# Performance work log

Measured on AMD Instinct MI355X. Metric: run time of the kernel, lower is better.

## Reference

```python
import jax, jax.numpy as jnp
import numpy as np

E, B, S, D, F = 8, 8, 2048, 1024, 4096  # experts, batch, seq, d_model, d_expert
LANG_BASE = 4  # lang codes 4..11 map to experts 0..7 (codes <=3 are non-routed specials)


def setup_inputs() -> dict:
    key = jax.random.key(0)
    k = jax.random.split(key, 5)
    hidden_states = jax.random.normal(k[0], (B, S, D), jnp.float32)
    w1 = jax.random.normal(k[1], (E, D, F), jnp.float32) * (1.0 / np.sqrt(D))
    w3 = jax.random.normal(k[2], (E, D, F), jnp.float32) * (1.0 / np.sqrt(D))
    w2 = jax.random.normal(k[3], (E, F, D), jnp.float32) * (1.0 / np.sqrt(F))
    langs = jax.random.randint(k[4], (B, 1), LANG_BASE, LANG_BASE + E)
    return {"hidden_states": hidden_states, "w1": w1, "w2": w2, "w3": w3, "langs": langs}


def reference(hidden_states, w1, w2, w3, langs):
    # routing_weights = 1 / (#langs > 3 per row), with inf -> 1 when no routed lang
    cnt = (langs > 3).sum(axis=-1)
    rw = jnp.where(cnt == 0, 1.0, 1.0 / jnp.maximum(cnt, 1)).astype(hidden_states.dtype)
    # one lang per row -> exactly one expert per batch row; gather its weights
    e_idx = langs[:, 0] - LANG_BASE  # [B]
    W1 = w1[e_idx]  # [B, D, F]
    W3 = w3[e_idx]  # [B, D, F]
    W2 = w2[e_idx]  # [B, F, D]
    a = jnp.einsum('bsd,bdf->bsf', hidden_states, W1)
    b = jnp.einsum('bsd,bdf->bsf', hidden_states, W3)
    h = jax.nn.gelu(a, approximate=False) * b
    out = jnp.einsum('bsf,bfd->bsd', h, W2)
    return out * rw[:, None, None]
```

## Files before the change

kernel.cpp:

```cpp
#include <hip/hip_runtime.h>
#include <hip/hip_bf16.h>
#include <stdint.h>

#define E_ 8
#define B_ 8
#define S_ 2048
#define D_ 1024
#define F_ 4096

typedef short short8 __attribute__((ext_vector_type(8)));
typedef float f32x4  __attribute__((ext_vector_type(4)));
typedef unsigned short u16;

union U16x8 { uint4 v; u16 s[8]; };
union U16x4 { uint2 v; u16 s[4]; };

__device__ __forceinline__ float gelu_exact(float x) {
    return 0.5f * x * (1.0f + erff(x * 0.70710678118654752f));
}
__device__ __forceinline__ u16 f2b(float v) {
    __hip_bfloat16 b = __float2bfloat16(v);
    return *(const u16*)&b;
}

__device__ __forceinline__ void gload_lds16(const u16* g, u16* l) {
    __builtin_amdgcn_global_load_lds(
        (const __attribute__((address_space(1))) uint32_t*)g,
        (__attribute__((address_space(3))) uint32_t*)l, 16, 0, 0);
}

__global__ void convert_x(const float* __restrict__ X, u16* __restrict__ Xb) {
    const size_t i = ((size_t)blockIdx.x * 256 + threadIdx.x) * 8;
    const float4 v0 = *(const float4*)(X + i);
    const float4 v1 = *(const float4*)(X + i + 4);
    U16x8 o;
    o.s[0] = f2b(v0.x); o.s[1] = f2b(v0.y); o.s[2] = f2b(v0.z); o.s[3] = f2b(v0.w);
    o.s[4] = f2b(v1.x); o.s[5] = f2b(v1.y); o.s[6] = f2b(v1.z); o.s[7] = f2b(v1.w);
    *(uint4*)(Xb + i) = o.v;
}

__global__ void transpose_w(const float* __restrict__ src, u16* __restrict__ dst,
                            int R, int C) {
    __shared__ u16 tile[64 * 72];
    const int c0 = blockIdx.x * 64;
    const int r0 = blockIdx.y * 64;
    const size_t base = (size_t)blockIdx.z * R * C;
    const int t  = threadIdx.x;
    const int rr = t >> 4;
    const int cc = (t & 15) * 4;
#pragma unroll
    for (int p = 0; p < 4; ++p) {
        const int r = rr + p * 16;
        const float4 v = *(const float4*)(src + base + (size_t)(r0 + r) * C + c0 + cc);
        tile[(cc + 0) * 72 + r] = f2b(v.x);
        tile[(cc + 1) * 72 + r] = f2b(v.y);
        tile[(cc + 2) * 72 + r] = f2b(v.z);
        tile[(cc + 3) * 72 + r] = f2b(v.w);
    }
    __syncthreads();
    const int cn = t >> 2;
    const int ch = (t & 3) * 4;
#pragma unroll
    for (int p = 0; p < 4; ++p) {
        const int rch = ch + p * 16;
        *(uint2*)(dst + base + (size_t)(c0 + cn) * R + r0 + rch) =
            *(const uint2*)(tile + cn * 72 + rch);
    }
}

__global__ __launch_bounds__(256, 2)
void gateup_v2(const u16* __restrict__ Xb, const u16* __restrict__ W1t,
               const u16* __restrict__ W3t, const int* __restrict__ langs,
               u16* __restrict__ H)
{
    __shared__ u16 sX [128 * 64];
    __shared__ u16 sW1[ 64 * 64];
    __shared__ u16 sW3[ 64 * 64];

    const int f0 = blockIdx.x * 64;
    const int s0 = blockIdx.y * 128;
    const int b  = blockIdx.z;
    const int e  = (langs[b] - 4) & 7;

    const int t    = threadIdx.x;
    const int lane = t & 63;
    const int w    = t >> 6;
    const int wr   = w >> 1, wc = w & 1;
    const int lm   = lane & 15;
    const int lq   = lane >> 4;
    const int lr   = lane >> 3;
    const int lcg  = (lane & 7) ^ lr;
    const int hsw  = lm & 7;

    f32x4 acc1[4][2], acc2[4][2];
#pragma unroll
    for (int i = 0; i < 4; ++i)
#pragma unroll
        for (int j = 0; j < 2; ++j) {
            acc1[i][j] = (f32x4){0.f, 0.f, 0.f, 0.f};
            acc2[i][j] = (f32x4){0.f, 0.f, 0.f, 0.f};
        }

    const size_t xbase = ((size_t)b * S_ + s0) * D_;
    const size_t wbase = ((size_t)e * F_ + f0) * D_;
    const u16* xg  = Xb  + xbase + (size_t)(w * 32 + lr) * D_ + lcg * 8;
    const u16* w1g = W1t + wbase + (size_t)(w * 16 + lr) * D_ + lcg * 8;
    const u16* w3g = W3t + wbase + (size_t)(w * 16 + lr) * D_ + lcg * 8;

    for (int kt = 0; kt < D_ / 64; ++kt) {
        const int k0 = kt * 64;
        __syncthreads();
#pragma unroll
        for (int i = 0; i < 4; ++i)
            gload_lds16(xg + (size_t)i * 8 * D_ + k0, sX + (w * 32 + i * 8) * 64);
#pragma unroll
        for (int i = 0; i < 2; ++i) {
            gload_lds16(w1g + (size_t)i * 8 * D_ + k0, sW1 + (w * 16 + i * 8) * 64);
            gload_lds16(w3g + (size_t)i * 8 * D_ + k0, sW3 + (w * 16 + i * 8) * 64);
        }
        __syncthreads();

#pragma unroll
        for (int kk = 0; kk < 64; kk += 32) {
            const int cgb = kk >> 3;
            short8 a[4], b1[2], b3[2];
#pragma unroll
            for (int i = 0; i < 4; ++i) {
                const int r = wr * 64 + i * 16 + lm;
                a[i] = *(const short8*)(sX + r * 64 + (((cgb + lq) ^ hsw) << 3));
            }
#pragma unroll
            for (int j = 0; j < 2; ++j) {
                const int n = wc * 32 + j * 16 + lm;
                b1[j] = *(const short8*)(sW1 + n * 64 + (((cgb + lq) ^ hsw) << 3));
                b3[j] = *(const short8*)(sW3 + n * 64 + (((cgb + lq) ^ hsw) << 3));
            }
#pragma unroll
            for (int i = 0; i < 4; ++i)
#pragma unroll
                for (int j = 0; j < 2; ++j) {
                    acc1[i][j] = __builtin_amdgcn_mfma_f32_16x16x32_bf16(a[i], b1[j], acc1[i][j], 0, 0, 0);
                    acc2[i][j] = __builtin_amdgcn_mfma_f32_16x16x32_bf16(a[i], b3[j], acc2[i][j], 0, 0, 0);
                }
        }
    }

#pragma unroll
    for (int i = 0; i < 4; ++i)
#pragma unroll
        for (int j = 0; j < 2; ++j)
#pragma unroll
            for (int r = 0; r < 4; ++r) {
                const int row = wr * 64 + i * 16 + lq * 4 + r;
                const int col = wc * 32 + j * 16 + lm;
                const float hv = gelu_exact(acc1[i][j][r]) * acc2[i][j][r];
                H[((size_t)b * S_ + s0 + row) * F_ + f0 + col] = f2b(hv);
            }
}

__global__ __launch_bounds__(256, 2)
void down_v2(const u16* __restrict__ H, const u16* __restrict__ W2t,
             const int* __restrict__ langs, float* __restrict__ Y)
{
    __shared__ u16 sH[128 * 64];
    __shared__ u16 sW[128 * 64];

    const int d0 = blockIdx.x * 128;
    const int s0 = blockIdx.y * 128;
    const int b  = blockIdx.z;
    const int e  = (langs[b] - 4) & 7;

    const int t    = threadIdx.x;
    const int lane = t & 63;
    const int w    = t >> 6;
    const int wr   = w >> 1, wc = w & 1;
    const int lm   = lane & 15;
    const int lq   = lane >> 4;
    const int lr   = lane >> 3;
    const int lcg  = (lane & 7) ^ lr;
    const int hsw  = lm & 7;

    f32x4 acc[4][4];
#pragma unroll
    for (int i = 0; i < 4; ++i)
#pragma unroll
        for (int j = 0; j < 4; ++j) acc[i][j] = (f32x4){0.f, 0.f, 0.f, 0.f};

    const size_t hbase = ((size_t)b * S_ + s0) * F_;
    const size_t wbase = ((size_t)e * D_ + d0) * F_;
    const u16* hg = H   + hbase + (size_t)(w * 32 + lr) * F_ + lcg * 8;
    const u16* wg = W2t + wbase + (size_t)(w * 32 + lr) * F_ + lcg * 8;

    for (int kt = 0; kt < F_ / 64; ++kt) {
        const int k0 = kt * 64;
        __syncthreads();
#pragma unroll
        for (int i = 0; i < 4; ++i)
            gload_lds16(hg + (size_t)i * 8 * F_ + k0, sH + (w * 32 + i * 8) * 64);
#pragma unroll
        for (int i = 0; i < 4; ++i)
            gload_lds16(wg + (size_t)i * 8 * F_ + k0, sW + (w * 32 + i * 8) * 64);
        __syncthreads();

#pragma unroll
        for (int kk = 0; kk < 64; kk += 32) {
            const int cgb = kk >> 3;
            short8 a[4], bb[4];
#pragma unroll
            for (int i = 0; i < 4; ++i) {
                const int r = wr * 64 + i * 16 + lm;
                a[i] = *(const short8*)(sH + r * 64 + (((cgb + lq) ^ hsw) << 3));
            }
#pragma unroll
            for (int j = 0; j < 4; ++j) {
                const int n = wc * 64 + j * 16 + lm;
                bb[j] = *(const short8*)(sW + n * 64 + (((cgb + lq) ^ hsw) << 3));
            }
#pragma unroll
            for (int i = 0; i < 4; ++i)
#pragma unroll
                for (int j = 0; j < 4; ++j)
                    acc[i][j] = __builtin_amdgcn_mfma_f32_16x16x32_bf16(a[i], bb[j], acc[i][j], 0, 0, 0);
        }
    }

#pragma unroll
    for (int i = 0; i < 4; ++i)
#pragma unroll
        for (int j = 0; j < 4; ++j)
#pragma unroll
            for (int r = 0; r < 4; ++r) {
                const int row = wr * 64 + i * 16 + lq * 4 + r;
                const int col = wc * 64 + j * 16 + lm;
                Y[((size_t)b * S_ + s0 + row) * D_ + d0 + col] = acc[i][j][r];
            }
}

__device__ __forceinline__ U16x8 load8f(const float* p, size_t off) {
    U16x8 r;
    const float4 v0 = *(const float4*)(p + off);
    const float4 v1 = *(const float4*)(p + off + 4);
    r.s[0] = f2b(v0.x); r.s[1] = f2b(v0.y); r.s[2] = f2b(v0.z); r.s[3] = f2b(v0.w);
    r.s[4] = f2b(v1.x); r.s[5] = f2b(v1.y); r.s[6] = f2b(v1.z); r.s[7] = f2b(v1.w);
    return r;
}

__global__ __launch_bounds__(256, 2)
void gateup_fb(const float* __restrict__ X, const float* __restrict__ W1,
               const float* __restrict__ W3, const int* __restrict__ langs,
               u16* __restrict__ H, int s_off, int schunk)
{
    __shared__ u16 sX [128 * 72];
    __shared__ u16 sW1[ 64 * 72];
    __shared__ u16 sW3[ 64 * 72];
    const int f0 = blockIdx.x * 64;
    const int sl = blockIdx.y * 128;
    const int b  = blockIdx.z;
    const int e  = (langs[b] - 4) & 7;
    const int t = threadIdx.x, lane = t & 63, w = t >> 6;
    const int wr = w >> 1, wc = w & 1, lm = lane & 15, lq = lane >> 4;
    const int wsel = t >> 7, idx = t & 127;
    const int wn = (idx & 7) * 8, wk = (idx >> 3) * 4;
    const float* Wsrc = wsel ? W3 : W1;
    u16* sWdst = wsel ? sW3 : sW1;

    f32x4 acc1[4][2], acc2[4][2];
#pragma unroll
    for (int i = 0; i < 4; ++i)
#pragma unroll
        for (int j = 0; j < 2; ++j) {
            acc1[i][j] = (f32x4){0.f,0.f,0.f,0.f};
            acc2[i][j] = (f32x4){0.f,0.f,0.f,0.f};
        }
    const size_t xbase = ((size_t)b * S_ + s_off + sl) * D_;
    const size_t wbase = (size_t)e * D_ * F_ + f0;
    for (int kt = 0; kt < D_ / 64; ++kt) {
        const int k0 = kt * 64;
        U16x8 xr[4], rr[4];
#pragma unroll
        for (int i = 0; i < 4; ++i) {
            const int ch = t + i * 256, row = ch >> 3, kk = (ch & 7) * 8;
            xr[i] = load8f(X, xbase + (size_t)row * D_ + k0 + kk);
        }
#pragma unroll
        for (int r = 0; r < 4; ++r)
            rr[r] = load8f(Wsrc, wbase + (size_t)(k0 + wk + r) * F_ + wn);
        __syncthreads();
#pragma unroll
        for (int i = 0; i < 4; ++i) {
            const int ch = t + i * 256, row = ch >> 3, kk = (ch & 7) * 8;
            *(uint4*)(sX + row * 72 + kk) = xr[i].v;
        }
#pragma unroll
        for (int j = 0; j < 8; ++j) {
            U16x4 o;
            o.s[0] = rr[0].s[j]; o.s[1] = rr[1].s[j];
            o.s[2] = rr[2].s[j]; o.s[3] = rr[3].s[j];
            *(uint2*)(sWdst + (wn + j) * 72 + wk) = o.v;
        }
        __syncthreads();
#pragma unroll
        for (int kk = 0; kk < 64; kk += 32) {
            short8 a[4], b1[2], b3[2];
#pragma unroll
            for (int i = 0; i < 4; ++i)
                a[i] = *(const short8*)(sX + (wr * 64 + i * 16 + lm) * 72 + kk + lq * 8);
#pragma unroll
            for (int j = 0; j < 2; ++j) {
                b1[j] = *(const short8*)(sW1 + (wc * 32 + j * 16 + lm) * 72 + kk + lq * 8);
                b3[j] = *(const short8*)(sW3 + (wc * 32 + j * 16 + lm) * 72 + kk + lq * 8);
            }
#pragma unroll
            for (int i = 0; i < 4; ++i)
#pragma unroll
                for (int j = 0; j < 2; ++j) {
                    acc1[i][j] = __builtin_amdgcn_mfma_f32_16x16x32_bf16(a[i], b1[j], acc1[i][j], 0, 0, 0);
                    acc2[i][j] = __builtin_amdgcn_mfma_f32_16x16x32_bf16(a[i], b3[j], acc2[i][j], 0, 0, 0);
                }
        }
    }
#pragma unroll
    for (int i = 0; i < 4; ++i)
#pragma unroll
        for (int j = 0; j < 2; ++j)
#pragma unroll
            for (int r = 0; r < 4; ++r) {
                const int row = wr * 64 + i * 16 + lq * 4 + r;
                const int col = wc * 32 + j * 16 + lm;
                H[((size_t)b * schunk + sl + row) * F_ + f0 + col] =
                    f2b(gelu_exact(acc1[i][j][r]) * acc2[i][j][r]);
            }
}

__global__ __launch_bounds__(256, 2)
void down_fb(const u16* __restrict__ Hm, const float* __restrict__ W2,
             const int* __restrict__ langs, float* __restrict__ Y,
             int s_off, int schunk)
{
    __shared__ u16 sH[128 * 72];
    __shared__ u16 sW[128 * 72];
    const int d0 = blockIdx.x * 128;
    const int sl = blockIdx.y * 128;
    const int b  = blockIdx.z;
    const int e  = (langs[b] - 4) & 7;
    const int t = threadIdx.x, lane = t & 63, w = t >> 6;
    const int wr = w >> 1, wc = w & 1, lm = lane & 15, lq = lane >> 4;
    const int wn = (t & 15) * 8, wk = (t >> 4) * 4;

    f32x4 acc[4][4];
#pragma unroll
    for (int i = 0; i < 4; ++i)
#pragma unroll
        for (int j = 0; j < 4; ++j) acc[i][j] = (f32x4){0.f,0.f,0.f,0.f};
    const size_t hbase = ((size_t)b * schunk + sl) * F_;
    const size_t wbase = (size_t)e * F_ * D_ + d0;
    for (int kt = 0; kt < F_ / 64; ++kt) {
        const int k0 = kt * 64;
        U16x8 hr[4], rr[4];
#pragma unroll
        for (int i = 0; i < 4; ++i) {
            const int ch = t + i * 256, row = ch >> 3, kk = (ch & 7) * 8;
            hr[i].v = *(const uint4*)(Hm + hbase + (size_t)row * F_ + k0 + kk);
        }
#pragma unroll
        for (int r = 0; r < 4; ++r)
            rr[r] = load8f(W2, wbase + (size_t)(k0 + wk + r) * D_ + wn);
        __syncthreads();
#pragma unroll
        for (int i = 0; i < 4; ++i) {
            const int ch = t + i * 256, row = ch >> 3, kk = (ch & 7) * 8;
            *(uint4*)(sH + row * 72 + kk) = hr[i].v;
        }
#pragma unroll
        for (int j = 0; j < 8; ++j) {
            U16x4 o;
            o.s[0] = rr[0].s[j]; o.s[1] = rr[1].s[j];
            o.s[2] = rr[2].s[j]; o.s[3] = rr[3].s[j];
            *(uint2*)(sW + (wn + j) * 72 + wk) = o.v;
        }
        __syncthreads();
#pragma unroll
        for (int kk = 0; kk < 64; kk += 32) {
            short8 a[4], bb[4];
#pragma unroll
            for (int i = 0; i < 4; ++i)
                a[i] = *(const short8*)(sH + (wr * 64 + i * 16 + lm) * 72 + kk + lq * 8);
#pragma unroll
            for (int j = 0; j < 4; ++j)
                bb[j] = *(const short8*)(sW + (wc * 64 + j * 16 + lm) * 72 + kk + lq * 8);
#pragma unroll
            for (int i = 0; i < 4; ++i)
#pragma unroll
                for (int j = 0; j < 4; ++j)
                    acc[i][j] = __builtin_amdgcn_mfma_f32_16x16x32_bf16(a[i], bb[j], acc[i][j], 0, 0, 0);
        }
    }
#pragma unroll
    for (int i = 0; i < 4; ++i)
#pragma unroll
        for (int j = 0; j < 4; ++j)
#pragma unroll
            for (int r = 0; r < 4; ++r) {
                const int row = wr * 64 + i * 16 + lq * 4 + r;
                const int col = wc * 64 + j * 16 + lm;
                Y[((size_t)b * S_ + s_off + sl + row) * D_ + d0 + col] = acc[i][j][r];
            }
}

extern "C" void kernel_launch(void* const* d_in, const int* in_sizes, int n_in,
                              void* d_out, int out_size, void* d_ws, size_t ws_size,
                              hipStream_t stream) {
    const float* X  = (const float*)d_in[0];
    const float* W1 = (const float*)d_in[1];
    const float* W2 = (const float*)d_in[2];
    const float* W3 = (const float*)d_in[3];
    const int* langs = (const int*)d_in[4];
    float* Y = (float*)d_out;

    const size_t szXb = (size_t)B_ * S_ * D_ * 2;
    const size_t szW  = (size_t)E_ * F_ * D_ * 2;
    const size_t szH  = (size_t)B_ * S_ * F_ * 2;
    const size_t need = szXb + 2 * szW + szH;

    if (ws_size >= need) {
        u16* Xb  = (u16*)d_ws;
        u16* W1t = (u16*)((char*)d_ws + szXb);
        u16* W3t = (u16*)((char*)d_ws + szXb + szW);
        u16* W2t = W1t;
        u16* Hb  = (u16*)((char*)d_ws + szXb + 2 * szW);

        convert_x<<<(B_ * S_ * D_) / (256 * 8), 256, 0, stream>>>(X, Xb);
        dim3 gt1(F_ / 64, D_ / 64, E_);
        transpose_w<<<gt1, 256, 0, stream>>>(W1, W1t, D_, F_);
        transpose_w<<<gt1, 256, 0, stream>>>(W3, W3t, D_, F_);
        dim3 g1(F_ / 64, S_ / 128, B_);
        gateup_v2<<<g1, 256, 0, stream>>>(Xb, W1t, W3t, langs, Hb);
        dim3 gt2(D_ / 64, F_ / 64, E_);
        transpose_w<<<gt2, 256, 0, stream>>>(W2, W2t, F_, D_);
        dim3 g2(D_ / 128, S_ / 128, B_);
        down_v2<<<g2, 256, 0, stream>>>(Hb, W2t, langs, Y);
    } else {
        u16* H = (u16*)d_ws;
        const size_t slab = (size_t)B_ * F_ * 2 * 128;
        int nslabs = (int)(ws_size / slab);
        if (nslabs < 1) nslabs = 1;
        if (nslabs > S_ / 128) nslabs = S_ / 128;
        const int SCH = nslabs * 128;
        for (int s0 = 0; s0 < S_; s0 += SCH) {
            const int rows = (S_ - s0 < SCH) ? (S_ - s0) : SCH;
            dim3 g1(F_ / 64, rows / 128, B_);
            gateup_fb<<<g1, 256, 0, stream>>>(X, W1, W3, langs, H, s0, SCH);
            dim3 g2(D_ / 128, rows / 128, B_);
            down_fb<<<g2, 256, 0, stream>>>(H, W2, langs, Y, s0, SCH);
        }
    }
}
```

Measured before the change: 867.9 us.

## Rewrite gate-up and down GEMMs with larger tiles and double-buffered LDS pipeline

After: 890.0 us. 1.03x slower.

```diff
diff --git a/kernel.cpp b/kernel.cpp
--- a/kernel.cpp
+++ b/kernel.cpp
@@ -28,6 +28,12 @@
         (const __attribute__((address_space(1))) uint32_t*)g,
         (__attribute__((address_space(3))) uint32_t*)l, 16, 0, 0);
 }
+
+#define SBAR asm volatile("s_barrier" ::: "memory")
+#define WLG0 asm volatile("s_waitcnt lgkmcnt(0)" ::: "memory")
+#define WVM8 asm volatile("s_waitcnt vmcnt(8)" ::: "memory")
+#define WVM4 asm volatile("s_waitcnt vmcnt(4)" ::: "memory")
+#define WVM0 asm volatile("s_waitcnt vmcnt(0)" ::: "memory")
 
 __global__ void convert_x(const float* __restrict__ X, u16* __restrict__ Xb) {
     const size_t i = ((size_t)blockIdx.x * 256 + threadIdx.x) * 8;
@@ -68,17 +74,15 @@
     }
 }
 
-__global__ __launch_bounds__(256, 2)
-void gateup_v2(const u16* __restrict__ Xb, const u16* __restrict__ W1t,
+
+__global__ __launch_bounds__(512, 2)
+void gateup_v3(const u16* __restrict__ Xb, const u16* __restrict__ W1t,
                const u16* __restrict__ W3t, const int* __restrict__ langs,
                u16* __restrict__ H)
 {
-    __shared__ u16 sX [128 * 64];
-    __shared__ u16 sW1[ 64 * 64];
-    __shared__ u16 sW3[ 64 * 64];
-
-    const int f0 = blockIdx.x * 64;
-    const int s0 = blockIdx.y * 128;
+    __shared__ u16 lds[65536];
+    const int f0 = blockIdx.x * 128;
+    const int s0 = blockIdx.y * 256;
     const int b  = blockIdx.z;
     const int e  = (langs[b] - 4) & 7;
 
@@ -86,154 +90,205 @@
     const int lane = t & 63;
     const int w    = t >> 6;
     const int wr   = w >> 1, wc = w & 1;
-    const int lm   = lane & 15;
-    const int lq   = lane >> 4;
-    const int lr   = lane >> 3;
-    const int lcg  = (lane & 7) ^ lr;
-    const int hsw  = lm & 7;
-
-    f32x4 acc1[4][2], acc2[4][2];
+    const int lm   = lane & 15, lq = lane >> 4;
+    const int sr   = lane >> 2, sg = lane & 3;
+
+    const u16* xg   = Xb + ((size_t)b * S_ + s0 + w * 32 + sr) * D_ + sg * 8;
+    const u16* bsrc = (w < 4 ? W1t : W3t)
+                    + ((size_t)e * F_ + f0 + (w & 3) * 32 + sr) * D_ + sg * 8;
+    const int aofs = w * 1024;
+    const int bofs = 16384 + (w >> 2) * 4096 + (w & 3) * 1024;
+
+    f32x4 acc1[4][4], acc2[4][4];
 #pragma unroll
     for (int i = 0; i < 4; ++i)
 #pragma unroll
-        for (int j = 0; j < 2; ++j) {
+        for (int j = 0; j < 4; ++j) {
             acc1[i][j] = (f32x4){0.f, 0.f, 0.f, 0.f};
             acc2[i][j] = (f32x4){0.f, 0.f, 0.f, 0.f};
         }
-
-    const size_t xbase = ((size_t)b * S_ + s0) * D_;
-    const size_t wbase = ((size_t)e * F_ + f0) * D_;
-    const u16* xg  = Xb  + xbase + (size_t)(w * 32 + lr) * D_ + lcg * 8;
-    const u16* w1g = W1t + wbase + (size_t)(w * 16 + lr) * D_ + lcg * 8;
-    const u16* w3g = W3t + wbase + (size_t)(w * 16 + lr) * D_ + lcg * 8;
-
-    for (int kt = 0; kt < D_ / 64; ++kt) {
-        const int k0 = kt * 64;
-        __syncthreads();
-#pragma unroll
-        for (int i = 0; i < 4; ++i)
-            gload_lds16(xg + (size_t)i * 8 * D_ + k0, sX + (w * 32 + i * 8) * 64);
-#pragma unroll
-        for (int i = 0; i < 2; ++i) {
-            gload_lds16(w1g + (size_t)i * 8 * D_ + k0, sW1 + (w * 16 + i * 8) * 64);
-            gload_lds16(w3g + (size_t)i * 8 * D_ + k0, sW3 + (w * 16 + i * 8) * 64);
-        }
-        __syncthreads();
-
-#pragma unroll
-        for (int kk = 0; kk < 64; kk += 32) {
-            const int cgb = kk >> 3;
-            short8 a[4], b1[2], b3[2];
-#pragma unroll
-            for (int i = 0; i < 4; ++i) {
-                const int r = wr * 64 + i * 16 + lm;
-                a[i] = *(const short8*)(sX + r * 64 + (((cgb + lq) ^ hsw) << 3));
+    short8 a[2], b1[4], b3[4];
+
+#define GU_STA(bf, kh, kt) do { \
+    gload_lds16(xg + (size_t)(kt) * 64 + (kh) * 32, \
+                lds + (bf) * 32768 + (kh) * 8192 + aofs); \
+    gload_lds16(xg + (size_t)16 * D_ + (size_t)(kt) * 64 + (kh) * 32, \
+                lds + (bf) * 32768 + (kh) * 8192 + aofs + 512); } while (0)
+#define GU_STB(bf, kh, kt) do { \
+    gload_lds16(bsrc + (size_t)(kt) * 64 + (kh) * 32, \
+                lds + (bf) * 32768 + (kh) * 8192 + bofs); \
+    gload_lds16(bsrc + (size_t)16 * D_ + (size_t)(kt) * 64 + (kh) * 32, \
+                lds + (bf) * 32768 + (kh) * 8192 + bofs + 512); } while (0)
+#define GU_RD(bf, kh, qi, LOADB) do { \
+    const u16* ab_ = lds + (bf) * 32768 + (kh) * 8192; \
+    _Pragma("unroll") \
+    for (int i2 = 0; i2 < 2; ++i2) \
+        a[i2] = *(const short8*)(ab_ + (wr * 64 + (qi) * 32 + i2 * 16 + lm) * 32 + lq * 8); \
+    if (LOADB) { \
+        const u16* bb_ = ab_ + 16384; \
+        _Pragma("unroll") \
+        for (int j = 0; j < 4; ++j) { \
+            b1[j] = *(const short8*)(bb_ + (wc * 64 + j * 16 + lm) * 32 + lq * 8); \
+            b3[j] = *(const short8*)(bb_ + 4096 + (wc * 64 + j * 16 + lm) * 32 + lq * 8); \
+        } } } while (0)
+#define GU_MM(qi) do { \
+    __builtin_amdgcn_s_setprio(1); \
+    _Pragma("unroll") \
+    for (int i2 = 0; i2 < 2; ++i2) \
+    _Pragma("unroll") \
+    for (int j = 0; j < 4; ++j) { \
+        acc1[(qi)*2 + i2][j] = __builtin_amdgcn_mfma_f32_16x16x32_bf16(a[i2], b1[j], acc1[(qi)*2 + i2][j], 0, 0, 0); \
+        acc2[(qi)*2 + i2][j] = __builtin_amdgcn_mfma_f32_16x16x32_bf16(a[i2], b3[j], acc2[(qi)*2 + i2][j], 0, 0, 0); \
+    } \
+    __builtin_amdgcn_s_setprio(0); } while (0)
+#define GU_PH(bf, kh, qi, LOADB, STG, WT) do { \
+    GU_RD(bf, kh, qi, LOADB); STG; SBAR; GU_MM(qi); WT; WLG0; SBAR; } while (0)
+
+    GU_STA(0, 0, 0); GU_STB(0, 0, 0);
+    GU_STA(0, 1, 0); GU_STB(0, 1, 0);
+    GU_STA(1, 0, 1); GU_STB(1, 0, 1);
+    WVM8; SBAR;
+
+#pragma unroll 1
+    for (int u = 0; u < D_ / 128 - 1; ++u) {
+        const int T1 = 2 * u + 1, TN = 2 * u + 2;
+        GU_PH(0, 0, 0, 1, GU_STA(1, 1, T1), );
+        GU_PH(0, 0, 1, 0, GU_STB(1, 1, T1), WVM8);
+        GU_PH(0, 1, 0, 1, GU_STA(0, 0, TN), );
+        GU_PH(0, 1, 1, 0, GU_STB(0, 0, TN), WVM8);
+        GU_PH(1, 0, 0, 1, GU_STA(0, 1, TN), );
+        GU_PH(1, 0, 1, 0, GU_STB(0, 1, TN), WVM8);
+        GU_PH(1, 1, 0, 1, GU_STA(1, 0, TN + 1), );
+        GU_PH(1, 1, 1, 0, GU_STB(1, 0, TN + 1), WVM8);
+    }
+    GU_PH(0, 0, 0, 1, GU_STA(1, 1, D_ / 64 - 1), );
+    GU_PH(0, 0, 1, 0, GU_STB(1, 1, D_ / 64 - 1), WVM8);
+    GU_PH(0, 1, 0, 1, , );
+    GU_PH(0, 1, 1, 0, , WVM4);
+    GU_PH(1, 0, 0, 1, , );
+    GU_PH(1, 0, 1, 0, , WVM0);
+    GU_PH(1, 1, 0, 1, , );
+    GU_PH(1, 1, 1, 0, , );
+
+#pragma unroll
+    for (int fi = 0; fi < 4; ++fi)
+#pragma unroll
+        for (int j = 0; j < 4; ++j)
+#pragma unroll
+            for (int r = 0; r < 4; ++r) {
+                const int row = s0 + wr * 64 + fi * 16 + lq * 4 + r;
+                const int col = f0 + wc * 64 + j * 16 + lm;
+                H[((size_t)b * S_ + row) * F_ + col] =
+                    f2b(gelu_exact(acc1[fi][j][r]) * acc2[fi][j][r]);
             }
-#pragma unroll
-            for (int j = 0; j < 2; ++j) {
-                const int n = wc * 32 + j * 16 + lm;
-                b1[j] = *(const short8*)(sW1 + n * 64 + (((cgb + lq) ^ hsw) << 3));
-                b3[j] = *(const short8*)(sW3 + n * 64 + (((cgb + lq) ^ hsw) << 3));
-            }
-#pragma unroll
-            for (int i = 0; i < 4; ++i)
-#pragma unroll
-                for (int j = 0; j < 2; ++j) {
-                    acc1[i][j] = __builtin_amdgcn_mfma_f32_16x16x32_bf16(a[i], b1[j], acc1[i][j], 0, 0, 0);
-                    acc2[i][j] = __builtin_amdgcn_mfma_f32_16x16x32_bf16(a[i], b3[j], acc2[i][j], 0, 0, 0);
-                }
-        }
-    }
-
-#pragma unroll
-    for (int i = 0; i < 4; ++i)
-#pragma unroll
-        for (int j = 0; j < 2; ++j)
-#pragma unroll
-            for (int r = 0; r < 4; ++r) {
-                const int row = wr * 64 + i * 16 + lq * 4 + r;
-                const int col = wc * 32 + j * 16 + lm;
-                const float hv = gelu_exact(acc1[i][j][r]) * acc2[i][j][r];
-                H[((size_t)b * S_ + s0 + row) * F_ + f0 + col] = f2b(hv);
-            }
-}
-
-__global__ __launch_bounds__(256, 2)
-void down_v2(const u16* __restrict__ H, const u16* __restrict__ W2t,
+#undef GU_STA
+#undef GU_STB
+#undef GU_RD
+#undef GU_MM
+#undef GU_PH
+}
+
+__global__ __launch_bounds__(512, 2)
+void down_v3(const u16* __restrict__ H, const u16* __restrict__ W2t,
              const int* __restrict__ langs, float* __restrict__ Y)
 {
-    __shared__ u16 sH[128 * 64];
-    __shared__ u16 sW[128 * 64];
-
-    const int d0 = blockIdx.x * 128;
-    const int s0 = blockIdx.y * 128;
+    __shared__ u16 lds[65536];
+    const int d0 = blockIdx.x * 256;
+    const int s0 = blockIdx.y * 256;
     const int b  = blockIdx.z;
     const int e  = (langs[b] - 4) & 7;
 
     const int t    = threadIdx.x;
     const int lane = t & 63;
     const int w    = t >> 6;
-    const int wr   = w >> 1, wc = w & 1;
-    const int lm   = lane & 15;
-    const int lq   = lane >> 4;
-    const int lr   = lane >> 3;
-    const int lcg  = (lane & 7) ^ lr;
-    const int hsw  = lm & 7;
-
-    f32x4 acc[4][4];
-#pragma unroll
-    for (int i = 0; i < 4; ++i)
+    const int wr   = w >> 2, wc = w & 3;
+    const int lm   = lane & 15, lq = lane >> 4;
+    const int sr   = lane >> 2, sg = lane & 3;
+
+    const u16* ha = H   + ((size_t)b * S_ + s0 + w * 32 + sr) * F_ + sg * 8;
+    const u16* wa = W2t + ((size_t)e * D_ + d0 + w * 32 + sr) * F_ + sg * 8;
+    const int aofs = w * 1024;
+
+    f32x4 acc[8][4];
+#pragma unroll
+    for (int i = 0; i < 8; ++i)
 #pragma unroll
         for (int j = 0; j < 4; ++j) acc[i][j] = (f32x4){0.f, 0.f, 0.f, 0.f};
-
-    const size_t hbase = ((size_t)b * S_ + s0) * F_;
-    const size_t wbase = ((size_t)e * D_ + d0) * F_;
-    const u16* hg = H   + hbase + (size_t)(w * 32 + lr) * F_ + lcg * 8;
-    const u16* wg = W2t + wbase + (size_t)(w * 32 + lr) * F_ + lcg * 8;
-
-    for (int kt = 0; kt < F_ / 64; ++kt) {
-        const int k0 = kt * 64;
-        __syncthreads();
-#pragma unroll
-        for (int i = 0; i < 4; ++i)
-            gload_lds16(hg + (size_t)i * 8 * F_ + k0, sH + (w * 32 + i * 8) * 64);
-#pragma unroll
-        for (int i = 0; i < 4; ++i)
-            gload_lds16(wg + (size_t)i * 8 * F_ + k0, sW + (w * 32 + i * 8) * 64);
-        __syncthreads();
-
-#pragma unroll
-        for (int kk = 0; kk < 64; kk += 32) {
-            const int cgb = kk >> 3;
-            short8 a[4], bb[4];
-#pragma unroll
-            for (int i = 0; i < 4; ++i) {
-                const int r = wr * 64 + i * 16 + lm;
-                a[i] = *(const short8*)(sH + r * 64 + (((cgb + lq) ^ hsw) << 3));
+    short8 a[4], bb[4];
+
+#define DN_STA(bf, kh, kt) do { \
+    gload_lds16(ha + (size_t)(kt) * 64 + (kh) * 32, \
+                lds + (bf) * 32768 + (kh) * 8192 + aofs); \
+    gload_lds16(ha + (size_t)16 * F_ + (size_t)(kt) * 64 + (kh) * 32, \
+                lds + (bf) * 32768 + (kh) * 8192 + aofs + 512); } while (0)
+#define DN_STB(bf, kh, kt) do { \
+    gload_lds16(wa + (size_t)(kt) * 64 + (kh) * 32, \
+                lds + (bf) * 32768 + 16384 + (kh) * 8192 + aofs); \
+    gload_lds16(wa + (size_t)16 * F_ + (size_t)(kt) * 64 + (kh) * 32, \
+                lds + (bf) * 32768 + 16384 + (kh) * 8192 + aofs + 512); } while (0)
+#define DN_RD(bf, kh, qi, LOADB) do { \
+    const u16* ab_ = lds + (bf) * 32768 + (kh) * 8192; \
+    _Pragma("unroll") \
+    for (int i = 0; i < 4; ++i) \
+        a[i] = *(const short8*)(ab_ + (wr * 128 + (qi) * 64 + i * 16 + lm) * 32 + lq * 8); \
+    if (LOADB) { \
+        const u16* bb_ = ab_ + 16384; \
+        _Pragma("unroll") \
+        for (int j = 0; j < 4; ++j) \
+            bb[j] = *(const short8*)(bb_ + (wc * 64 + j * 16 + lm) * 32 + lq * 8); \
+    } } while (0)
+#define DN_MM(qi) do { \
+    __builtin_amdgcn_s_setprio(1); \
+    _Pragma("unroll") \
+    for (int i = 0; i < 4; ++i) \
+    _Pragma("unroll") \
+    for (int j = 0; j < 4; ++j) \
+        acc[(qi)*4 + i][j] = __builtin_amdgcn_mfma_f32_16x16x32_bf16(a[i], bb[j], acc[(qi)*4 + i][j], 0, 0, 0); \
+    __builtin_amdgcn_s_setprio(0); } while (0)
+#define DN_PH(bf, kh, qi, LOADB, STG, WT) do { \
+    DN_RD(bf, kh, qi, LOADB); STG; SBAR; DN_MM(qi); WT; WLG0; SBAR; } while (0)
+
+    DN_STA(0, 0, 0); DN_STB(0, 0, 0);
+    DN_STA(0, 1, 0); DN_STB(0, 1, 0);
+    DN_STA(1, 0, 1); DN_STB(1, 0, 1);
+    WVM8; SBAR;
+
+#pragma unroll 1
+    for (int u = 0; u < F_ / 128 - 1; ++u) {
+        const int T1 = 2 * u + 1, TN = 2 * u + 2;
+        DN_PH(0, 0, 0, 1, DN_STA(1, 1, T1), );
+        DN_PH(0, 0, 1, 0, DN_STB(1, 1, T1), WVM8);
+        DN_PH(0, 1, 0, 1, DN_STA(0, 0, TN), );
+        DN_PH(0, 1, 1, 0, DN_STB(0, 0, TN), WVM8);
+        DN_PH(1, 0, 0, 1, DN_STA(0, 1, TN), );
+        DN_PH(1, 0, 1, 0, DN_STB(0, 1, TN), WVM8);
+        DN_PH(1, 1, 0, 1, DN_STA(1, 0, TN + 1), );
+        DN_PH(1, 1, 1, 0, DN_STB(1, 0, TN + 1), WVM8);
+    }
+    DN_PH(0, 0, 0, 1, DN_STA(1, 1, F_ / 64 - 1), );
+    DN_PH(0, 0, 1, 0, DN_STB(1, 1, F_ / 64 - 1), WVM8);
+    DN_PH(0, 1, 0, 1, , );
+    DN_PH(0, 1, 1, 0, , WVM4);
+    DN_PH(1, 0, 0, 1, , );
+    DN_PH(1, 0, 1, 0, , WVM0);
+    DN_PH(1, 1, 0, 1, , );
+    DN_PH(1, 1, 1, 0, , );
+
+#pragma unroll
+    for (int fi = 0; fi < 8; ++fi)
+#pragma unroll
+        for (int j = 0; j < 4; ++j)
+#pragma unroll
+            for (int r = 0; r < 4; ++r) {
+                const int row = s0 + wr * 128 + fi * 16 + lq * 4 + r;
+                const int col = d0 + wc * 64 + j * 16 + lm;
+                Y[((size_t)b * S_ + row) * D_ + col] = acc[fi][j][r];
             }
-#pragma unroll
-            for (int j = 0; j < 4; ++j) {
-                const int n = wc * 64 + j * 16 + lm;
-                bb[j] = *(const short8*)(sW + n * 64 + (((cgb + lq) ^ hsw) << 3));
-            }
-#pragma unroll
-            for (int i = 0; i < 4; ++i)
-#pragma unroll
-                for (int j = 0; j < 4; ++j)
-                    acc[i][j] = __builtin_amdgcn_mfma_f32_16x16x32_bf16(a[i], bb[j], acc[i][j], 0, 0, 0);
-        }
-    }
-
-#pragma unroll
-    for (int i = 0; i < 4; ++i)
-#pragma unroll
-        for (int j = 0; j < 4; ++j)
-#pragma unroll
-            for (int r = 0; r < 4; ++r) {
-                const int row = wr * 64 + i * 16 + lq * 4 + r;
-                const int col = wc * 64 + j * 16 + lm;
-                Y[((size_t)b * S_ + s0 + row) * D_ + d0 + col] = acc[i][j][r];
-            }
+#undef DN_STA
+#undef DN_STB
+#undef DN_RD
+#undef DN_MM
+#undef DN_PH
 }
 
 __device__ __forceinline__ U16x8 load8f(const float* p, size_t off) {
@@ -433,12 +488,12 @@
         dim3 gt1(F_ / 64, D_ / 64, E_);
         transpose_w<<<gt1, 256, 0, stream>>>(W1, W1t, D_, F_);
         transpose_w<<<gt1, 256, 0, stream>>>(W3, W3t, D_, F_);
-        dim3 g1(F_ / 64, S_ / 128, B_);
-        gateup_v2<<<g1, 256, 0, stream>>>(Xb, W1t, W3t, langs, Hb);
+        dim3 g1(F_ / 128, S_ / 256, B_);
+        gateup_v3<<<g1, 512, 0, stream>>>(Xb, W1t, W3t, langs, Hb);
         dim3 gt2(D_ / 64, F_ / 64, E_);
         transpose_w<<<gt2, 256, 0, stream>>>(W2, W2t, F_, D_);
-        dim3 g2(D_ / 128, S_ / 128, B_);
-        down_v2<<<g2, 256, 0, stream>>>(Hb, W2t, langs, Y);
+        dim3 g2(D_ / 256, S_ / 256, B_);
+        down_v3<<<g2, 512, 0, stream>>>(Hb, W2t, langs, Y);
     } else {
         u16* H = (u16*)d_ws;
         const size_t slab = (size_t)B_ * F_ * 2 * 128;
```
